# Performance work log

Measured on AMD Instinct MI355X. Metric: run time of the kernel, lower is better.

Reference implementation:

```python
import jax, jax.numpy as jnp
import numpy as np

B, S, D = 2048, 200, 128  # batch, history length, embedding dim
H = 64                    # attention_units[0]

def setup_inputs() -> dict:
    key = jax.random.key(0)
    k1, k2, k3, k4, k5 = jax.random.split(key, 5)
    return {
        "target_item": jax.random.normal(k1, (B, D), dtype=jnp.float32),
        "history_sequence": jax.random.normal(k2, (B, S, D), dtype=jnp.float32),
        "mask": jax.random.randint(k3, (B, S), 0, 2, dtype=jnp.int32),
        "W1": jax.random.normal(k4, (4 * D, H), dtype=jnp.float32) * (1.0 / np.sqrt(4 * D)),
        "b1": jnp.zeros((H,), dtype=jnp.float32),
        "W2": jax.random.normal(k5, (H, 1), dtype=jnp.float32) * (1.0 / np.sqrt(H)),
        "b2": jnp.zeros((1,), dtype=jnp.float32),
    }

def reference(target_item, history_sequence, mask, W1, b1, W2, b2):
    b, s, d = history_sequence.shape
    t = jnp.broadcast_to(target_item[:, None, :], (b, s, d))  # [B,S,D]
    # concat(target, history, diff, product) -> [B,S,4D]
    x = jnp.concatenate(
        [t, history_sequence, t - history_sequence, t * history_sequence], axis=-1)
    h = jax.nn.relu(x @ W1 + b1)          # [B,S,H]
    w = (h @ W2 + b2)[..., 0]             # [B,S]
    m = mask.astype(w.dtype)
    w = w * m                              # zero out padded positions (pre-softmax, as in source)
    w = w + (-1e9) * (1.0 - m)             # mask for softmax
    w = jax.nn.softmax(w, axis=-1)
    return jnp.einsum('bs,bsd->bd', w, history_sequence)  # [B,D]
```

## Files before the change

kernel.cpp:

```cpp
#include <hip/hip_runtime.h>
#include <hip/hip_bf16.h>

typedef __attribute__((ext_vector_type(8))) short bf16x8;
typedef __attribute__((ext_vector_type(4))) float f32x4;

#define B_ 2048
#define S_ 200
#define D_ 128
#define H_ 64
#define LOG2E 1.44269504f
#define TR 14
#define TB (TR*512)

#define WS_TA 0u
#define WS_AC (512u*1024u)
#define WS_BC (512u*1024u + 32768u)
#define WS_DT (512u*1024u + 65536u)
#define WS_CN (512u*1024u + 98304u)
#define WS_LS (512u*1024u + 106496u)

#define L_LIST 16384
#define L_BUF  17408

static __device__ __forceinline__ short f2bf_hw(float f) {
    return (short)__builtin_bit_cast(unsigned short, __float2bfloat16(f));
}

static __device__ __forceinline__ void gload16(const void* g, void* l) {
    __builtin_amdgcn_global_load_lds(
        (const __attribute__((address_space(1))) unsigned int*)g,
        (__attribute__((address_space(3))) unsigned int*)l, 16, 0, 0);
}

__global__ __launch_bounds__(128)
void prep_fold(const float* __restrict__ W1, char* __restrict__ ws)
{
    const int n = blockIdx.x;
    const int k = threadIdx.x;
    float a = W1[k * H_ + n];
    float b = W1[(128 + k) * H_ + n];
    float c = W1[(256 + k) * H_ + n];
    float d = W1[(384 + k) * H_ + n];
    ((float*)(ws + WS_AC))[n * 128 + k] = a + c;
    ((float*)(ws + WS_BC))[n * 128 + k] = b - c;
    ((float*)(ws + WS_DT))[n * 128 + k] = d;
}

__global__ __launch_bounds__(256)
void prep_ta(const float* __restrict__ tgt, const float* __restrict__ b1,
             char* __restrict__ ws)
{
    __shared__ float tl[4][128];
    const int tid = threadIdx.x;
    const int b0 = blockIdx.x * 4;
    if (tid < 128) {
        int bb = tid >> 5, q = tid & 31;
        *(float4*)&tl[bb][q * 4] = ((const float4*)(tgt + (size_t)(b0 + bb) * D_))[q];
    }
    __syncthreads();
    const int n = tid & 63, bb = tid >> 6;
    const float* ac = (const float*)(ws + WS_AC) + n * 128;
    float s = 0.f;
    #pragma unroll 8
    for (int d = 0; d < 128; ++d) s = fmaf(tl[bb][d], ac[d], s);
    ((float*)(ws + WS_TA))[(size_t)(b0 + bb) * H_ + n] = s + b1[n];
}

__global__ __launch_bounds__(256)
void mask_build(const int* __restrict__ mask, char* __restrict__ ws)
{
    const int lane = threadIdx.x & 63;
    const int wv   = threadIdx.x >> 6;
    const int b    = blockIdx.x * 4 + wv;
    const int* mp  = mask + (size_t)b * S_;
    int* lst = (int*)(ws + WS_LS) + (size_t)b * 208;
    int cnt = 0, last = 0;
    #pragma unroll
    for (int c = 0; c < 4; ++c) {
        int s = c * 64 + lane;
        int m = (s < S_) ? mp[s] : 0;
        unsigned long long bal = __ballot(m != 0);
        if (m) lst[cnt + __builtin_popcountll(bal & ((1ull << lane) - 1ull))] = s;
        if (bal) last = c * 64 + (63 - __builtin_clzll(bal));
        cnt += __builtin_popcountll(bal);
    }
    int uni = 0;
    if (cnt == 0) { uni = 1; cnt = S_; }
    for (int p = cnt + lane; p < 208; p += 64) lst[p] = uni ? (S_ - 1) : last;
    if (uni)
        for (int p = lane; p < S_; p += 64) lst[p] = p;
    if (lane == 0) ((int*)(ws + WS_CN))[b] = cnt | (uni << 16);
}

__global__ __launch_bounds__(256) __attribute__((amdgpu_waves_per_eu(2, 2)))
void din_fused(const float* __restrict__ tgt, const float* __restrict__ hist,
               const float* __restrict__ W2, const char* __restrict__ ws,
               float* __restrict__ out)
{
    __shared__ __align__(16) char L[L_BUF + 4 * 2 * TB];
    const int tid  = threadIdx.x;
    const int lane = tid & 63;
    const int wv   = tid >> 6;
    const int b    = blockIdx.x;
    const int lo   = lane & 15;
    const int hi   = lane >> 4;

    const int cw  = ((const int*)(ws + WS_CN))[b];
    const int cnt = cw & 0xffff;
    const int uni = cw >> 16;
    const int nt  = (cnt + TR - 1) / TR;

    if (tid < 52)
        ((int4*)(L + L_LIST))[tid] = ((const int4*)(ws + WS_LS + (size_t)b * 832u))[tid];

    f32x4 tav[4], w2v[4];
    #pragma unroll
    for (int ng = 0; ng < 4; ++ng) {
        tav[ng] = *(const f32x4*)((const float*)(ws + WS_TA) + (size_t)b * H_ + ng * 16 + hi * 4);
        f32x4 wl = *(const f32x4*)(W2 + ng * 16 + hi * 4);
        w2v[ng] = (f32x4){wl[0] * LOG2E, wl[1] * LOG2E, wl[2] * LOG2E, wl[3] * LOG2E};
    }

    {
        const float* bcT = (const float*)(ws + WS_BC);
        const float* dT  = (const float*)(ws + WS_DT);
        const int kb = tid & 15;
        f32x4 t0 = *(const f32x4*)(tgt + (size_t)b * D_ + kb * 8);
        f32x4 t1 = *(const f32x4*)(tgt + (size_t)b * D_ + kb * 8 + 4);
        #pragma unroll
        for (int j = 0; j < 4; ++j) {
            int n = (tid >> 4) + j * 16;
            f32x4 bc0 = *(const f32x4*)(bcT + n * 128 + kb * 8);
            f32x4 bc1 = *(const f32x4*)(bcT + n * 128 + kb * 8 + 4);
            f32x4 dd0 = *(const f32x4*)(dT  + n * 128 + kb * 8);
            f32x4 dd1 = *(const f32x4*)(dT  + n * 128 + kb * 8 + 4);
            bf16x8 v;
            #pragma unroll
            for (int e = 0; e < 4; ++e) {
                v[e]     = f2bf_hw(fmaf(t0[e], dd0[e], bc0[e]));
                v[e + 4] = f2bf_hw(fmaf(t1[e], dd1[e], bc1[e]));
            }
            *(bf16x8*)(L + n * 256 + ((kb * 16) ^ ((n & 7) << 4))) = v;
        }
    }
    __syncthreads();

    int abase[4], akoff[4];
    #pragma unroll
    for (int ng = 0; ng < 4; ++ng) abase[ng] = (ng * 16 + lo) * 256;
    #pragma unroll
    for (int ks = 0; ks < 4; ++ks) akoff[ks] = (ks * 64 + hi * 16) ^ ((lo & 7) << 4);
    const int loc = lo > TR - 1 ? TR - 1 : lo;
    const int rb  = (loc * 512 + hi * 32) ^ ((loc & 7) << 4);
    const int prb = (loc * 512 + wv * 0 + hi * 32) ^ ((loc & 7) << 4);
    char* B0 = L + L_BUF + wv * (2 * TB);
    char* B1 = B0 + TB;

    const char* hb = (const char*)hist + (size_t)b * (S_ * D_ * 4);
    const int cp = (lane & 31) * 16;
    const int h5 = lane >> 5;
    const int* ll = (const int*)(L + L_LIST);

    auto stage_pos = [&](int t, char* bufp) {
        int rr[7];
        #pragma unroll
        for (int i = 0; i < 7; ++i) rr[i] = ll[t * TR + 2 * i + h5];
        #pragma unroll
        for (int i = 0; i < 7; ++i)
            gload16(hb + (size_t)rr[i] * 512 + (cp ^ (((2 * i + h5) & 7) << 4)),
                    bufp + i * 1024);
    };

    float o[4][8];
    #pragma unroll
    for (int ks = 0; ks < 4; ++ks)
        #pragma unroll
        for (int e = 0; e < 8; ++e) o[ks][e] = 0.f;
    float l = 0.f, mx = -1e30f;

    auto compt = [&](int t, char* buf, int nxt) {
        int r[7];
        if (nxt >= 0) {
            #pragma unroll
            for (int i = 0; i < 7; ++i) r[i] = ll[nxt * TR + 2 * i + h5];
        }
        f32x4 h0[4], h1[4];
        #pragma unroll
        for (int ks = 0; ks < 4; ++ks) {
            int o4 = rb + ks * 128;
            h0[ks] = *(const f32x4*)(buf + o4);
            h1[ks] = *(const f32x4*)(buf + (o4 ^ 16));
        }
        asm volatile("s_waitcnt lgkmcnt(0)" ::: "memory");
        __builtin_amdgcn_sched_barrier(0);
        if (nxt >= 0) {
            #pragma unroll
            for (int i = 0; i < 7; ++i)
                gload16(hb + (size_t)r[i] * 512 + (cp ^ (((2 * i + h5) & 7) << 4)),
                        buf + i * 1024);
        }
        f32x4 acc[4];
        #pragma unroll
        for (int ng = 0; ng < 4; ++ng) acc[ng] = (f32x4){0.f, 0.f, 0.f, 0.f};
        #pragma unroll
        for (int ks = 0; ks < 4; ++ks) {
            bf16x8 bfr;
            #pragma unroll
            for (int e = 0; e < 4; ++e) {
                bfr[e]     = f2bf_hw(h0[ks][e]);
                bfr[e + 4] = f2bf_hw(h1[ks][e]);
            }
            #pragma unroll
            for (int ng = 0; ng < 4; ++ng) {
                bf16x8 af = *(const bf16x8*)(L + abase[ng] + akoff[ks]);
                acc[ng] = __builtin_amdgcn_mfma_f32_16x16x32_bf16(af, bfr, acc[ng], 0, 0, 0);
            }
        }
        float s0 = 0.f, s1 = 0.f, s2 = 0.f, s3 = 0.f;
        #pragma unroll
        for (int e = 0; e < 4; ++e) {
            s0 = fmaf(fmaxf(acc[0][e] + tav[0][e], 0.f), w2v[0][e], s0);
            s1 = fmaf(fmaxf(acc[1][e] + tav[1][e], 0.f), w2v[1][e], s1);
            s2 = fmaf(fmaxf(acc[2][e] + tav[2][e], 0.f), w2v[2][e], s2);
            s3 = fmaf(fmaxf(acc[3][e] + tav[3][e], 0.f), w2v[3][e], s3);
        }
        float sum = (s0 + s1) + (s2 + s3);
        sum += __shfl_xor(sum, 16);
        sum += __shfl_xor(sum, 32);
        const bool valid = (t * TR + lo < cnt) && (lo < TR);
        float lg = uni ? (valid ? 0.f : -1e30f) : (valid ? sum : -1e30f);
        float tm = lg;
        tm = fmaxf(tm, __shfl_xor(tm, 1));
        tm = fmaxf(tm, __shfl_xor(tm, 2));
        tm = fmaxf(tm, __shfl_xor(tm, 4));
        tm = fmaxf(tm, __shfl_xor(tm, 8));
        if (tm > mx + 11.5f) {
            float rsc = exp2f(mx - tm);
            #pragma unroll
            for (int ks = 0; ks < 4; ++ks)
                #pragma unroll
                for (int e = 0; e < 8; ++e) o[ks][e] *= rsc;
            l *= rsc;
            mx = tm;
        }
        float p = valid ? exp2f(lg - mx) : 0.f;
        l += p;
        #pragma unroll
        for (int ks = 0; ks < 4; ++ks) {
            o[ks][0] = fmaf(p, h0[ks][0], o[ks][0]);
            o[ks][1] = fmaf(p, h0[ks][1], o[ks][1]);
            o[ks][2] = fmaf(p, h0[ks][2], o[ks][2]);
            o[ks][3] = fmaf(p, h0[ks][3], o[ks][3]);
            o[ks][4] = fmaf(p, h1[ks][0], o[ks][4]);
            o[ks][5] = fmaf(p, h1[ks][1], o[ks][5]);
            o[ks][6] = fmaf(p, h1[ks][2], o[ks][6]);
            o[ks][7] = fmaf(p, h1[ks][3], o[ks][7]);
        }
    };

    const int ntw = (nt > wv) ? ((nt - wv + 3) >> 2) : 0;
    if (ntw > 0) {
        stage_pos(wv, B0);
        if (ntw > 1) stage_pos(wv + 4, B1);
        #pragma unroll 1
        for (int j = 0; j + 2 < ntw; ++j) {
            char* bj = (j & 1) ? B1 : B0;
            asm volatile("s_waitcnt vmcnt(7)" ::: "memory");
            compt(wv + 4 * j, bj, wv + 4 * j + 8);
        }
        if (ntw >= 2) {
            char* bA = ((ntw - 2) & 1) ? B1 : B0;
            char* bB = ((ntw - 1) & 1) ? B1 : B0;
            asm volatile("s_waitcnt vmcnt(7)" ::: "memory");
            compt(wv + 4 * (ntw - 2), bA, -1);
            asm volatile("s_waitcnt vmcnt(0)" ::: "memory");
            compt(wv + 4 * (ntw - 1), bB, -1);
        } else {
            asm volatile("s_waitcnt vmcnt(0)" ::: "memory");
            compt(wv, B0, -1);
        }
    }

    #pragma unroll
    for (int ks = 0; ks < 4; ++ks)
        #pragma unroll
        for (int e = 0; e < 8; ++e) {
            float v = o[ks][e];
            v += __shfl_xor(v, 1);
            v += __shfl_xor(v, 2);
            v += __shfl_xor(v, 4);
            v += __shfl_xor(v, 8);
            o[ks][e] = v;
        }
    l += __shfl_xor(l, 1);
    l += __shfl_xor(l, 2);
    l += __shfl_xor(l, 4);
    l += __shfl_xor(l, 8);

    float* mo = (float*)B0;
    if (lo == 0) {
        #pragma unroll
        for (int ks = 0; ks < 4; ++ks) {
            *(f32x4*)(mo + ks * 32 + hi * 8)     = (f32x4){o[ks][0], o[ks][1], o[ks][2], o[ks][3]};
            *(f32x4*)(mo + ks * 32 + hi * 8 + 4) = (f32x4){o[ks][4], o[ks][5], o[ks][6], o[ks][7]};
        }
        if (hi == 0) { mo[128] = mx; mo[129] = l; }
    }
    __syncthreads();

    if (tid < 128) {
        const float* m0 = (const float*)(L + L_BUF);
        const float* m1 = (const float*)(L + L_BUF + 2 * TB);
        const float* m2 = (const float*)(L + L_BUF + 4 * TB);
        const float* m3 = (const float*)(L + L_BUF + 6 * TB);
        float mstar = fmaxf(fmaxf(m0[128], m1[128]), fmaxf(m2[128], m3[128]));
        float f0 = exp2f(m0[128] - mstar), f1 = exp2f(m1[128] - mstar);
        float f2 = exp2f(m2[128] - mstar), f3 = exp2f(m3[128] - mstar);
        float num = m0[tid] * f0 + m1[tid] * f1 + m2[tid] * f2 + m3[tid] * f3;
        float den = m0[129] * f0 + m1[129] * f1 + m2[129] * f2 + m3[129] * f3;
        out[(size_t)b * D_ + tid] = num / den;
    }
}

extern "C" void kernel_launch(void* const* d_in, const int* in_sizes, int n_in,
                              void* d_out, int out_size, void* d_ws, size_t ws_size,
                              hipStream_t stream) {
    const float* tgt  = (const float*)d_in[0];
    const float* hist = (const float*)d_in[1];
    const int*   mask = (const int*)d_in[2];
    const float* W1   = (const float*)d_in[3];
    const float* b1   = (const float*)d_in[4];
    const float* W2   = (const float*)d_in[5];
    const float* b2   = (const float*)d_in[6];
    (void)b2;
    float* out = (float*)d_out;
    char* ws = (char*)d_ws;

    prep_fold<<<64, 128, 0, stream>>>(W1, ws);
    prep_ta<<<B_ / 4, 256, 0, stream>>>(tgt, b1, ws);
    mask_build<<<B_ / 4, 256, 0, stream>>>(mask, ws);
    din_fused<<<B_, 256, 0, stream>>>(tgt, hist, W2, ws, out);
}
```

Measured before the change: 58.78 us.

## Map one batch row per wave with a shared weight image and K=256 MFMA

Each wave now handles a whole batch row instead of four waves splitting one row, so the cross-wave softmax merge and its block barrier go away. The per-row folded weight (bc + t*d) is replaced by a single bf16 weight image with K=256, and history is fed to the MFMA as both h and t*h. Per-row metadata (target, the target-times-weight term, count and index list) is packed into one workspace record and brought in with async loads. Tiles shrink to 8 positions and the pipeline is reorganised. This trades twice the MFMA work per tile and a minimum of two tiles per row for less per-block setup and no merge step.

```diff
diff --git a/kernel.cpp b/kernel.cpp
--- a/kernel.cpp
+++ b/kernel.cpp
@@ -9,18 +9,12 @@
 #define D_ 128
 #define H_ 64
 #define LOG2E 1.44269504f
-#define TR 14
-#define TB (TR*512)
-
-#define WS_TA 0u
-#define WS_AC (512u*1024u)
-#define WS_BC (512u*1024u + 32768u)
-#define WS_DT (512u*1024u + 65536u)
-#define WS_CN (512u*1024u + 98304u)
-#define WS_LS (512u*1024u + 106496u)
-
-#define L_LIST 16384
-#define L_BUF  17408
+#define TR 8
+#define TB 4096
+
+#define WS_AC 0u
+#define WS_WB 32768u
+#define WS_MT 65536u
 
 static __device__ __forceinline__ short f2bf_hw(float f) {
     return (short)__builtin_bit_cast(unsigned short, __float2bfloat16(f));
@@ -42,8 +36,11 @@
     float c = W1[(256 + k) * H_ + n];
     float d = W1[(384 + k) * H_ + n];
     ((float*)(ws + WS_AC))[n * 128 + k] = a + c;
-    ((float*)(ws + WS_BC))[n * 128 + k] = b - c;
-    ((float*)(ws + WS_DT))[n * 128 + k] = d;
+    char* img = ws + WS_WB;
+    const int sw = (n & 7) << 4;
+    const int kk = k >> 3, e2 = (k & 7) * 2;
+    *(short*)(img + n * 512 + ((kk * 16) ^ sw) + e2)          = f2bf_hw(b - c);
+    *(short*)(img + n * 512 + (((16 + kk) * 16) ^ sw) + e2)   = f2bf_hw(d);
 }
 
 __global__ __launch_bounds__(256)
@@ -63,17 +60,19 @@
     float s = 0.f;
     #pragma unroll 8
     for (int d = 0; d < 128; ++d) s = fmaf(tl[bb][d], ac[d], s);
-    ((float*)(ws + WS_TA))[(size_t)(b0 + bb) * H_ + n] = s + b1[n];
+    ((float*)(ws + WS_MT + (size_t)(b0 + bb) * 2048u + 512u))[n] = s + b1[n];
 }
 
 __global__ __launch_bounds__(256)
-void mask_build(const int* __restrict__ mask, char* __restrict__ ws)
+void mask_build(const int* __restrict__ mask, const float* __restrict__ tgt,
+                char* __restrict__ ws)
 {
     const int lane = threadIdx.x & 63;
     const int wv   = threadIdx.x >> 6;
     const int b    = blockIdx.x * 4 + wv;
     const int* mp  = mask + (size_t)b * S_;
-    int* lst = (int*)(ws + WS_LS) + (size_t)b * 208;
+    char* mt = ws + WS_MT + (size_t)b * 2048u;
+    int* lst = (int*)(mt + 1024);
     int cnt = 0, last = 0;
     #pragma unroll
     for (int c = 0; c < 4; ++c) {
@@ -89,87 +88,79 @@
     for (int p = cnt + lane; p < 208; p += 64) lst[p] = uni ? (S_ - 1) : last;
     if (uni)
         for (int p = lane; p < S_; p += 64) lst[p] = p;
-    if (lane == 0) ((int*)(ws + WS_CN))[b] = cnt | (uni << 16);
+    if (lane == 0) *(int*)(mt + 768) = cnt | (uni << 16);
+    if (lane < 32) ((float4*)mt)[lane] = ((const float4*)(tgt + (size_t)b * D_))[lane];
 }
 
 __global__ __launch_bounds__(256) __attribute__((amdgpu_waves_per_eu(2, 2)))
-void din_fused(const float* __restrict__ tgt, const float* __restrict__ hist,
-               const float* __restrict__ W2, const char* __restrict__ ws,
-               float* __restrict__ out)
+void din_fused(const float* __restrict__ hist, const float* __restrict__ W2,
+               const char* __restrict__ ws, float* __restrict__ out)
 {
-    __shared__ __align__(16) char L[L_BUF + 4 * 2 * TB];
+    __shared__ __align__(16) char L[73728];
     const int tid  = threadIdx.x;
     const int lane = tid & 63;
     const int wv   = tid >> 6;
-    const int b    = blockIdx.x;
+    const int b    = blockIdx.x * 4 + wv;
     const int lo   = lane & 15;
     const int hi   = lane >> 4;
-
-    const int cw  = ((const int*)(ws + WS_CN))[b];
+    char* Lm = L + 32768 + wv * 10240;
+    char* B0 = Lm + 2048;
+    char* B1 = Lm + 6144;
+
+    f32x4 w2v[4];
+    #pragma unroll
+    for (int ng = 0; ng < 4; ++ng) {
+        f32x4 wl = *(const f32x4*)(W2 + ng * 16 + hi * 4);
+        w2v[ng] = (f32x4){wl[0] * LOG2E, wl[1] * LOG2E, wl[2] * LOG2E, wl[3] * LOG2E};
+    }
+
+    {
+        const char* wsrc = ws + WS_WB + wv * 8192 + (size_t)lane * 16u;
+        #pragma unroll
+        for (int i = 0; i < 8; ++i)
+            gload16(wsrc + i * 1024, L + wv * 8192 + i * 1024);
+        const char* msrc = ws + WS_MT + (size_t)b * 2048u + (size_t)lane * 16u;
+        gload16(msrc,        Lm);
+        gload16(msrc + 1024, Lm + 1024);
+    }
+    asm volatile("s_waitcnt vmcnt(0)" ::: "memory");
+    __syncthreads();
+
+    const int cw  = *(const int*)(Lm + 768);
     const int cnt = cw & 0xffff;
     const int uni = cw >> 16;
-    const int nt  = (cnt + TR - 1) / TR;
-
-    if (tid < 52)
-        ((int4*)(L + L_LIST))[tid] = ((const int4*)(ws + WS_LS + (size_t)b * 832u))[tid];
-
-    f32x4 tav[4], w2v[4];
-    #pragma unroll
-    for (int ng = 0; ng < 4; ++ng) {
-        tav[ng] = *(const f32x4*)((const float*)(ws + WS_TA) + (size_t)b * H_ + ng * 16 + hi * 4);
-        f32x4 wl = *(const f32x4*)(W2 + ng * 16 + hi * 4);
-        w2v[ng] = (f32x4){wl[0] * LOG2E, wl[1] * LOG2E, wl[2] * LOG2E, wl[3] * LOG2E};
-    }
-
-    {
-        const float* bcT = (const float*)(ws + WS_BC);
-        const float* dT  = (const float*)(ws + WS_DT);
-        const int kb = tid & 15;
-        f32x4 t0 = *(const f32x4*)(tgt + (size_t)b * D_ + kb * 8);
-        f32x4 t1 = *(const f32x4*)(tgt + (size_t)b * D_ + kb * 8 + 4);
-        #pragma unroll
-        for (int j = 0; j < 4; ++j) {
-            int n = (tid >> 4) + j * 16;
-            f32x4 bc0 = *(const f32x4*)(bcT + n * 128 + kb * 8);
-            f32x4 bc1 = *(const f32x4*)(bcT + n * 128 + kb * 8 + 4);
-            f32x4 dd0 = *(const f32x4*)(dT  + n * 128 + kb * 8);
-            f32x4 dd1 = *(const f32x4*)(dT  + n * 128 + kb * 8 + 4);
-            bf16x8 v;
-            #pragma unroll
-            for (int e = 0; e < 4; ++e) {
-                v[e]     = f2bf_hw(fmaf(t0[e], dd0[e], bc0[e]));
-                v[e + 4] = f2bf_hw(fmaf(t1[e], dd1[e], bc1[e]));
-            }
-            *(bf16x8*)(L + n * 256 + ((kb * 16) ^ ((n & 7) << 4))) = v;
-        }
-    }
-    __syncthreads();
-
-    int abase[4], akoff[4];
-    #pragma unroll
-    for (int ng = 0; ng < 4; ++ng) abase[ng] = (ng * 16 + lo) * 256;
-    #pragma unroll
-    for (int ks = 0; ks < 4; ++ks) akoff[ks] = (ks * 64 + hi * 16) ^ ((lo & 7) << 4);
-    const int loc = lo > TR - 1 ? TR - 1 : lo;
-    const int rb  = (loc * 512 + hi * 32) ^ ((loc & 7) << 4);
-    const int prb = (loc * 512 + wv * 0 + hi * 32) ^ ((loc & 7) << 4);
-    char* B0 = L + L_BUF + wv * (2 * TB);
-    char* B1 = B0 + TB;
+    int nt = (cnt + TR - 1) / TR; if (nt < 2) nt = 2;
+    const int* ll = (const int*)(Lm + 1024);
+
+    f32x4 tav[4];
+    #pragma unroll
+    for (int ng = 0; ng < 4; ++ng)
+        tav[ng] = *(const f32x4*)(Lm + 512 + (ng * 16 + hi * 4) * 4);
+
+    int abase[4], akoff[8];
+    #pragma unroll
+    for (int ng = 0; ng < 4; ++ng) abase[ng] = (ng * 16 + lo) * 512;
+    #pragma unroll
+    for (int ks = 0; ks < 8; ++ks) akoff[ks] = (ks * 64 + hi * 16) ^ ((lo & 7) << 4);
+    const int rb   = ((lo & 7) * 512 + hi * 32) ^ ((lo & 7) << 4);
+    const int toff = hi * 32;
 
     const char* hb = (const char*)hist + (size_t)b * (S_ * D_ * 4);
     const int cp = (lane & 31) * 16;
     const int h5 = lane >> 5;
-    const int* ll = (const int*)(L + L_LIST);
-
-    auto stage_pos = [&](int t, char* bufp) {
-        int rr[7];
-        #pragma unroll
-        for (int i = 0; i < 7; ++i) rr[i] = ll[t * TR + 2 * i + h5];
-        #pragma unroll
-        for (int i = 0; i < 7; ++i)
-            gload16(hb + (size_t)rr[i] * 512 + (cp ^ (((2 * i + h5) & 7) << 4)),
-                    bufp + i * 1024);
-    };
+
+    {
+        #pragma unroll
+        for (int i = 0; i < 4; ++i) {
+            int r = 2 * i + h5;
+            gload16(hb + (size_t)ll[r] * 512 + (cp ^ ((r & 7) << 4)), B0 + i * 1024);
+        }
+        #pragma unroll
+        for (int i = 0; i < 4; ++i) {
+            int r = 2 * i + h5;
+            gload16(hb + (size_t)ll[8 + r] * 512 + (cp ^ ((r & 7) << 4)), B1 + i * 1024);
+        }
+    }
 
     float o[4][8];
     #pragma unroll
@@ -179,41 +170,38 @@
     float l = 0.f, mx = -1e30f;
 
     auto compt = [&](int t, char* buf, int nxt) {
-        int r[7];
+        int r[4];
         if (nxt >= 0) {
             #pragma unroll
-            for (int i = 0; i < 7; ++i) r[i] = ll[nxt * TR + 2 * i + h5];
-        }
-        f32x4 h0[4], h1[4];
+            for (int i = 0; i < 4; ++i) r[i] = ll[nxt * TR + 2 * i + h5];
+        }
+        f32x4 acc[4];
+        #pragma unroll
+        for (int ng = 0; ng < 4; ++ng) acc[ng] = (f32x4){0.f, 0.f, 0.f, 0.f};
         #pragma unroll
         for (int ks = 0; ks < 4; ++ks) {
             int o4 = rb + ks * 128;
-            h0[ks] = *(const f32x4*)(buf + o4);
-            h1[ks] = *(const f32x4*)(buf + (o4 ^ 16));
-        }
-        asm volatile("s_waitcnt lgkmcnt(0)" ::: "memory");
-        __builtin_amdgcn_sched_barrier(0);
-        if (nxt >= 0) {
-            #pragma unroll
-            for (int i = 0; i < 7; ++i)
-                gload16(hb + (size_t)r[i] * 512 + (cp ^ (((2 * i + h5) & 7) << 4)),
-                        buf + i * 1024);
-        }
-        f32x4 acc[4];
-        #pragma unroll
-        for (int ng = 0; ng < 4; ++ng) acc[ng] = (f32x4){0.f, 0.f, 0.f, 0.f};
-        #pragma unroll
-        for (int ks = 0; ks < 4; ++ks) {
-            bf16x8 bfr;
+            f32x4 h0  = *(const f32x4*)(buf + o4);
+            f32x4 h1  = *(const f32x4*)(buf + (o4 ^ 16));
+            f32x4 tp0 = *(const f32x4*)(Lm + ks * 128 + toff);
+            f32x4 tp1 = *(const f32x4*)(Lm + ks * 128 + toff + 16);
+            bf16x8 bh, bt;
             #pragma unroll
             for (int e = 0; e < 4; ++e) {
-                bfr[e]     = f2bf_hw(h0[ks][e]);
-                bfr[e + 4] = f2bf_hw(h1[ks][e]);
+                bh[e]     = f2bf_hw(h0[e]);
+                bh[e + 4] = f2bf_hw(h1[e]);
+                bt[e]     = f2bf_hw(tp0[e] * h0[e]);
+                bt[e + 4] = f2bf_hw(tp1[e] * h1[e]);
             }
             #pragma unroll
             for (int ng = 0; ng < 4; ++ng) {
                 bf16x8 af = *(const bf16x8*)(L + abase[ng] + akoff[ks]);
-                acc[ng] = __builtin_amdgcn_mfma_f32_16x16x32_bf16(af, bfr, acc[ng], 0, 0, 0);
+                acc[ng] = __builtin_amdgcn_mfma_f32_16x16x32_bf16(af, bh, acc[ng], 0, 0, 0);
+            }
+            #pragma unroll
+            for (int ng = 0; ng < 4; ++ng) {
+                bf16x8 af = *(const bf16x8*)(L + abase[ng] + akoff[ks + 4]);
+                acc[ng] = __builtin_amdgcn_mfma_f32_16x16x32_bf16(af, bt, acc[ng], 0, 0, 0);
             }
         }
         float s0 = 0.f, s1 = 0.f, s2 = 0.f, s3 = 0.f;
@@ -247,38 +235,35 @@
         l += p;
         #pragma unroll
         for (int ks = 0; ks < 4; ++ks) {
-            o[ks][0] = fmaf(p, h0[ks][0], o[ks][0]);
-            o[ks][1] = fmaf(p, h0[ks][1], o[ks][1]);
-            o[ks][2] = fmaf(p, h0[ks][2], o[ks][2]);
-            o[ks][3] = fmaf(p, h0[ks][3], o[ks][3]);
-            o[ks][4] = fmaf(p, h1[ks][0], o[ks][4]);
-            o[ks][5] = fmaf(p, h1[ks][1], o[ks][5]);
-            o[ks][6] = fmaf(p, h1[ks][2], o[ks][6]);
-            o[ks][7] = fmaf(p, h1[ks][3], o[ks][7]);
+            int o4 = rb + ks * 128;
+            f32x4 h0 = *(const f32x4*)(buf + o4);
+            f32x4 h1 = *(const f32x4*)(buf + (o4 ^ 16));
+            o[ks][0] = fmaf(p, h0[0], o[ks][0]);
+            o[ks][1] = fmaf(p, h0[1], o[ks][1]);
+            o[ks][2] = fmaf(p, h0[2], o[ks][2]);
+            o[ks][3] = fmaf(p, h0[3], o[ks][3]);
+            o[ks][4] = fmaf(p, h1[0], o[ks][4]);
+            o[ks][5] = fmaf(p, h1[1], o[ks][5]);
+            o[ks][6] = fmaf(p, h1[2], o[ks][6]);
+            o[ks][7] = fmaf(p, h1[3], o[ks][7]);
+        }
+        asm volatile("s_waitcnt lgkmcnt(0)" ::: "memory");
+        __builtin_amdgcn_sched_barrier(0);
+        if (nxt >= 0) {
+            #pragma unroll
+            for (int i = 0; i < 4; ++i)
+                gload16(hb + (size_t)r[i] * 512 + (cp ^ (((2 * i + h5) & 7) << 4)),
+                        buf + i * 1024);
         }
     };
 
-    const int ntw = (nt > wv) ? ((nt - wv + 3) >> 2) : 0;
-    if (ntw > 0) {
-        stage_pos(wv, B0);
-        if (ntw > 1) stage_pos(wv + 4, B1);
-        #pragma unroll 1
-        for (int j = 0; j + 2 < ntw; ++j) {
-            char* bj = (j & 1) ? B1 : B0;
-            asm volatile("s_waitcnt vmcnt(7)" ::: "memory");
-            compt(wv + 4 * j, bj, wv + 4 * j + 8);
-        }
-        if (ntw >= 2) {
-            char* bA = ((ntw - 2) & 1) ? B1 : B0;
-            char* bB = ((ntw - 1) & 1) ? B1 : B0;
-            asm volatile("s_waitcnt vmcnt(7)" ::: "memory");
-            compt(wv + 4 * (ntw - 2), bA, -1);
-            asm volatile("s_waitcnt vmcnt(0)" ::: "memory");
-            compt(wv + 4 * (ntw - 1), bB, -1);
-        } else {
-            asm volatile("s_waitcnt vmcnt(0)" ::: "memory");
-            compt(wv, B0, -1);
-        }
+    #pragma unroll 1
+    for (int t = 0; t < nt; ++t) {
+        char* buf = (t & 1) ? B1 : B0;
+        if (t + 1 < nt) { asm volatile("s_waitcnt vmcnt(4)" ::: "memory"); }
+        else            { asm volatile("s_waitcnt vmcnt(0)" ::: "memory"); }
+        __builtin_amdgcn_sched_barrier(0);
+        compt(t, buf, (t + 2 < nt) ? t + 2 : -1);
     }
 
     #pragma unroll
@@ -297,28 +282,16 @@
     l += __shfl_xor(l, 4);
     l += __shfl_xor(l, 8);
 
-    float* mo = (float*)B0;
+    const float inv = 1.0f / l;
     if (lo == 0) {
+        float* op = out + (size_t)b * D_ + hi * 8;
         #pragma unroll
         for (int ks = 0; ks < 4; ++ks) {
-            *(f32x4*)(mo + ks * 32 + hi * 8)     = (f32x4){o[ks][0], o[ks][1], o[ks][2], o[ks][3]};
-            *(f32x4*)(mo + ks * 32 + hi * 8 + 4) = (f32x4){o[ks][4], o[ks][5], o[ks][6], o[ks][7]};
-        }
-        if (hi == 0) { mo[128] = mx; mo[129] = l; }
-    }
-    __syncthreads();
-
-    if (tid < 128) {
-        const float* m0 = (const float*)(L + L_BUF);
-        const float* m1 = (const float*)(L + L_BUF + 2 * TB);
-        const float* m2 = (const float*)(L + L_BUF + 4 * TB);
-        const float* m3 = (const float*)(L + L_BUF + 6 * TB);
-        float mstar = fmaxf(fmaxf(m0[128], m1[128]), fmaxf(m2[128], m3[128]));
-        float f0 = exp2f(m0[128] - mstar), f1 = exp2f(m1[128] - mstar);
-        float f2 = exp2f(m2[128] - mstar), f3 = exp2f(m3[128] - mstar);
-        float num = m0[tid] * f0 + m1[tid] * f1 + m2[tid] * f2 + m3[tid] * f3;
-        float den = m0[129] * f0 + m1[129] * f1 + m2[129] * f2 + m3[129] * f3;
-        out[(size_t)b * D_ + tid] = num / den;
+            *(f32x4*)(op + ks * 32)     = (f32x4){o[ks][0] * inv, o[ks][1] * inv,
+                                                  o[ks][2] * inv, o[ks][3] * inv};
+            *(f32x4*)(op + ks * 32 + 4) = (f32x4){o[ks][4] * inv, o[ks][5] * inv,
+                                                  o[ks][6] * inv, o[ks][7] * inv};
+        }
     }
 }
 
@@ -338,6 +311,6 @@
 
     prep_fold<<<64, 128, 0, stream>>>(W1, ws);
     prep_ta<<<B_ / 4, 256, 0, stream>>>(tgt, b1, ws);
-    mask_build<<<B_ / 4, 256, 0, stream>>>(mask, ws);
-    din_fused<<<B_, 256, 0, stream>>>(tgt, hist, W2, ws, out);
-}
+    mask_build<<<B_ / 4, 256, 0, stream>>>(mask, tgt, ws);
+    din_fused<<<B_ / 4, 256, 0, stream>>>(hist, W2, ws, out);
+}
```

Result: no change. 57.72 us (-1.8%).
